# Kernel optimization log

Hardware: AMD Instinct MI355X
Metric: run time of the kernel (lower is better)

## Reference

```python
import jax, jax.numpy as jnp
import numpy as np

K = 1024
H = 16
HEAD = K // H

def setup_inputs() -> dict:
    key = jax.random.key(0)
    ks = jax.random.split(key, 6)
    b, t = 2, 2048
    x = jax.random.normal(ks[0], (b, t, K), dtype=jnp.float32)
    padding = jnp.ones((b, t), dtype=jnp.int32)
    s = 1.0 / np.sqrt(K)
    Wq = jax.random.normal(ks[1], (K, K), dtype=jnp.float32) * s
    Wk = jax.random.normal(ks[2], (K, K), dtype=jnp.float32) * s
    Wv = jax.random.normal(ks[3], (K, K), dtype=jnp.float32) * s
    Wo = jax.random.normal(ks[4], (K, K), dtype=jnp.float32) * s
    bo = jnp.zeros((K,), dtype=jnp.float32)
    return {"x": x, "padding": padding, "Wq": Wq, "Wk": Wk, "Wv": Wv, "Wo": Wo, "bo": bo}

def reference(x, padding, Wq, Wk, Wv, Wo, bo):
    b, t, k = x.shape
    h, d = H, HEAD
    # projections (nn.Linear: x @ W.T), then split heads -> [b,h,t,d]
    q = (x @ Wq.T).reshape(b, t, h, d).transpose(0, 2, 1, 3)
    kk = (x @ Wk.T).reshape(b, t, h, d).transpose(0, 2, 1, 3)
    v = (x @ Wv.T).reshape(b, t, h, d).transpose(0, 2, 1, 3)
    scores = jnp.einsum('bhqd,bhkd->bhqk', q, kk)
    # key-side padding mask: positions with padding==0 get -inf (before scaling,
    # same result since -inf/sqrt(d) == -inf)
    mask = (padding == 0)[:, None, None, :]  # [b,1,1,t]
    scores = jnp.where(mask, -jnp.inf, scores) / np.sqrt(d).astype(np.float32)
    weights = jax.nn.softmax(scores, axis=-1)
    out = jnp.einsum('bhqk,bhkd->bhqd', weights, v)
    out = out.transpose(0, 2, 1, 3).reshape(b, t, h * d)
    return out @ Wo.T + bo
```

## Files before the change

### kernel.cpp

```cpp
#include <hip/hip_runtime.h>
#include <cmath>
#include <stdint.h>

#define K_DIM 1024
#define NH    16
#define HD    64
#define T     2048
#define NTOK  4096
#define NBH   32

typedef __bf16 bf16x8 __attribute__((ext_vector_type(8)));
typedef float  f32x4  __attribute__((ext_vector_type(4)));

__device__ __forceinline__ unsigned short f2bf(float f) {
  union { float f; unsigned u; } v; v.f = f;
  unsigned u = v.u;
  return (unsigned short)((u + 0x7FFFu + ((u >> 16) & 1u)) >> 16);
}
__device__ __forceinline__ unsigned short f2bf_hu(float f) {
  union { float f; unsigned u; } v; v.f = f;
  return (unsigned short)((v.u + 0x8000u) >> 16);
}

__device__ __forceinline__ void gload16(const void* g, void* l) {
  __builtin_amdgcn_global_load_lds(
      (__attribute__((address_space(1))) void*)(g),
      (__attribute__((address_space(3))) void*)(l),
      16, 0, 0);
}

__global__ void convert_kernel(const float* __restrict__ x,
                               const float* __restrict__ Wq,
                               const float* __restrict__ Wk,
                               const float* __restrict__ Wv,
                               const float* __restrict__ Wo,
                               unsigned short* __restrict__ xb,
                               unsigned short* __restrict__ wqkv,
                               unsigned short* __restrict__ wob)
{
  const size_t NX = (size_t)NTOK * K_DIM;
  const size_t NW = (size_t)K_DIM * K_DIM;
  size_t i = ((size_t)blockIdx.x * blockDim.x + threadIdx.x) * 4;
  const float* src; unsigned short* dst; size_t off;
  float scale = 1.f;
  if (i < NX)             { src = x;  dst = xb;          off = i; }
  else if (i < NX + NW)   { src = Wq; dst = wqkv;        off = i - NX;
                            scale = 0.18033688011112042f; }
  else if (i < NX + 2*NW) { src = Wk; dst = wqkv + NW;   off = i - NX - NW; }
  else if (i < NX + 3*NW) { src = Wv; dst = wqkv + 2*NW; off = i - NX - 2*NW; }
  else                    { src = Wo; dst = wob;         off = i - NX - 3*NW; }
  float4 v = *(const float4*)(src + off);
  ushort4 o;
  o.x = f2bf(v.x * scale); o.y = f2bf(v.y * scale);
  o.z = f2bf(v.z * scale); o.w = f2bf(v.w * scale);
  *(ushort4*)(dst + off) = o;
}

template <int MODE, int TM, int TN>
__global__ __launch_bounds__(256, 2)
void gemm_bt(const unsigned short* __restrict__ A,
             const unsigned short* __restrict__ B,
             unsigned short* __restrict__ o_q,
             unsigned short* __restrict__ o_k,
             unsigned short* __restrict__ o_v,
             float* __restrict__ o_f,
             const float* __restrict__ bias)
{
  __shared__ unsigned short Asm[TM * 64];
  __shared__ unsigned short Bsm[TN * 64];
  const int tid  = threadIdx.x;
  const int wave = tid >> 6;
  const int lane = tid & 63;
  const int lq   = lane & 15;
  const int quad = lane >> 4;
  const int bm = blockIdx.x, bn = blockIdx.y;
  const int wm = (wave >> 1) * (TM / 2), wn = (wave & 1) * (TN / 2);
  const int MT = TM / 32, NT = TN / 32;

  f32x4 acc[MT][NT];
#pragma unroll
  for (int i = 0; i < MT; ++i)
#pragma unroll
    for (int j = 0; j < NT; ++j) acc[i][j] = (f32x4){0.f, 0.f, 0.f, 0.f};

  const char* Ab = (const char*)(A + (size_t)bm * TM * K_DIM);
  const char* Bb = (const char*)(B + (size_t)bn * TN * K_DIM);

  for (int k0 = 0; k0 < K_DIM; k0 += 64) {
#pragma unroll
    for (int i = 0; i < MT; ++i) {
      int off   = i * 4096 + wave * 1024 + lane * 16;
      int row   = off >> 7;
      int chunk = (off >> 4) & 7;
      int scol  = (chunk ^ (row & 7)) << 4;
      gload16(Ab + (size_t)row * (K_DIM * 2) + (size_t)k0 * 2 + scol,
              (char*)Asm + off - lane * 16);
    }
#pragma unroll
    for (int i = 0; i < NT; ++i) {
      int off   = i * 4096 + wave * 1024 + lane * 16;
      int row   = off >> 7;
      int chunk = (off >> 4) & 7;
      int scol  = (chunk ^ (row & 7)) << 4;
      gload16(Bb + (size_t)row * (K_DIM * 2) + (size_t)k0 * 2 + scol,
              (char*)Bsm + off - lane * 16);
    }
    __syncthreads();
#pragma unroll
    for (int kk = 0; kk < 64; kk += 32) {
      bf16x8 af[MT], bfr[NT];
#pragma unroll
      for (int mt = 0; mt < MT; ++mt) {
        int row = wm + mt * 16 + lq;
        int sw  = (quad + (kk >> 3)) ^ (row & 7);
        af[mt] = *(const bf16x8*)((const char*)Asm + row * 128 + (sw << 4));
      }
#pragma unroll
      for (int nt = 0; nt < NT; ++nt) {
        int row = wn + nt * 16 + lq;
        int sw  = (quad + (kk >> 3)) ^ (row & 7);
        bfr[nt] = *(const bf16x8*)((const char*)Bsm + row * 128 + (sw << 4));
      }
#pragma unroll
      for (int mt = 0; mt < MT; ++mt)
#pragma unroll
        for (int nt = 0; nt < NT; ++nt)
          acc[mt][nt] = __builtin_amdgcn_mfma_f32_16x16x32_bf16(af[mt], bfr[nt], acc[mt][nt], 0, 0, 0);
    }
    __syncthreads();
  }

#pragma unroll
  for (int mt = 0; mt < MT; ++mt) {
    int mbase = bm * TM + wm + mt * 16 + quad * 4;
#pragma unroll
    for (int nt = 0; nt < NT; ++nt) {
      int n = bn * TN + wn + nt * 16 + lq;
      if (MODE == 1) {
        int which = mbase >> 10, c = mbase & 1023;
        int h = c >> 6, d0 = c & 63;
        int b = n >> 11, t = n & 2047;
        if (which < 2) {
          ushort4 pk;
          pk.x = f2bf(acc[mt][nt][0]); pk.y = f2bf(acc[mt][nt][1]);
          pk.z = f2bf(acc[mt][nt][2]); pk.w = f2bf(acc[mt][nt][3]);
          unsigned short* dst = which ? o_k : o_q;
          *(ushort4*)&dst[((size_t)(b * NH + h) * T + t) * HD + d0] = pk;
        } else {
#pragma unroll
          for (int r = 0; r < 4; ++r)
            o_v[((size_t)(b * NH + h) * HD + d0 + r) * T + t] = f2bf(acc[mt][nt][r]);
        }
      } else {
        float4 bv = *(const float4*)&bias[mbase];
        float4 o;
        o.x = acc[mt][nt][0] + bv.x; o.y = acc[mt][nt][1] + bv.y;
        o.z = acc[mt][nt][2] + bv.z; o.w = acc[mt][nt][3] + bv.w;
        *(float4*)&o_f[(size_t)n * K_DIM + mbase] = o;
      }
    }
  }
}

__global__ __launch_bounds__(256, 2)
void attn_kernel(const unsigned short* __restrict__ Q,
                 const unsigned short* __restrict__ Kb,
                 const unsigned short* __restrict__ Vt,
                 const int* __restrict__ padding,
                 unsigned short* __restrict__ O)
{
  __shared__ unsigned short Ksm[128 * 64];
  __shared__ unsigned short Vsm[64 * 128];
  __shared__ unsigned short Plds[4][16 * 32 * 4];

  const int tid  = threadIdx.x;
  const int wave = tid >> 6;
  const int lane = tid & 63;
  const int lq   = lane & 15;
  const int quad = lane >> 4;
  const int bh = blockIdx.x;
  const int qt = blockIdx.y;
  const int b  = bh >> 4;
  const int h  = bh & 15;
  const int qbase = qt * 128 + wave * 32;

  bf16x8 qf[2][2];
#pragma unroll
  for (int nq = 0; nq < 2; ++nq)
#pragma unroll
    for (int kk = 0; kk < 2; ++kk)
      qf[nq][kk] = *(const bf16x8*)&Q[((size_t)bh * T + qbase + nq * 16 + lq) * HD + kk * 32 + quad * 8];

  f32x4 o_acc[4][2];
#pragma unroll
  for (int md = 0; md < 4; ++md)
#pragma unroll
    for (int nq = 0; nq < 2; ++nq) o_acc[md][nq] = (f32x4){0.f, 0.f, 0.f, 0.f};
  float l_part[2] = {0.f, 0.f};

  for (int kt = 0; kt < T / 128; ++kt) {
#pragma unroll
    for (int i = 0; i < 4; ++i) {
      int off = i * 4096 + wave * 1024 + lane * 16;
      {
        int row = off >> 7, chunk = (off >> 4) & 7;
        int scol = (chunk ^ (row & 7)) << 4;
        gload16((const char*)Kb + ((size_t)(bh * T + kt * 128 + row) * HD) * 2 + scol,
                (char*)Ksm + off - lane * 16);
      }
      {
        int row = off >> 8, chunk = (off >> 4) & 15;
        int scol = (chunk ^ (row & 15)) << 4;
        gload16((const char*)Vt + ((size_t)(bh * HD + row) * T + (size_t)kt * 128) * 2 + scol,
                (char*)Vsm + off - lane * 16);
      }
    }
    __syncthreads();

    f32x4 st[8][2];
#pragma unroll
    for (int nt = 0; nt < 8; ++nt)
#pragma unroll
      for (int nq = 0; nq < 2; ++nq) st[nt][nq] = (f32x4){0.f, 0.f, 0.f, 0.f};
#pragma unroll
    for (int kk = 0; kk < 2; ++kk) {
#pragma unroll
      for (int nt = 0; nt < 8; ++nt) {
        int row = nt * 16 + lq;
        int sw  = (quad + kk * 4) ^ (row & 7);
        bf16x8 kf = *(const bf16x8*)((const char*)Ksm + row * 128 + (sw << 4));
        st[nt][0] = __builtin_amdgcn_mfma_f32_16x16x32_bf16(kf, qf[0][kk], st[nt][0], 0, 0, 0);
        st[nt][1] = __builtin_amdgcn_mfma_f32_16x16x32_bf16(kf, qf[1][kk], st[nt][1], 0, 0, 0);
      }
    }

#pragma unroll
    for (int half = 0; half < 2; ++half) {
#pragma unroll
      for (int nt2 = 0; nt2 < 4; ++nt2) {
        int nt = half * 4 + nt2;
        int4 pd = *(const int4*)&padding[b * T + kt * 128 + nt * 16 + quad * 4];
#pragma unroll
        for (int nq = 0; nq < 2; ++nq) {
          float p0 = pd.x ? __builtin_amdgcn_exp2f(st[nt][nq][0]) : 0.f;
          float p1 = pd.y ? __builtin_amdgcn_exp2f(st[nt][nq][1]) : 0.f;
          float p2 = pd.z ? __builtin_amdgcn_exp2f(st[nt][nq][2]) : 0.f;
          float p3 = pd.w ? __builtin_amdgcn_exp2f(st[nt][nq][3]) : 0.f;
          l_part[nq] += (p0 + p1) + (p2 + p3);
          ushort4 pk;
          pk.x = f2bf_hu(p0); pk.y = f2bf_hu(p1); pk.z = f2bf_hu(p2); pk.w = f2bf_hu(p3);
          int row = nt2 * 4 + quad;
          int col = nq * 16 + lq;
          *(ushort4*)&Plds[wave][(row * 32 + col) * 4] = pk;
        }
      }
      asm volatile("s_waitcnt lgkmcnt(0)" ::: "memory");

#pragma unroll
      for (int kk2 = 0; kk2 < 2; ++kk2) {
        int kchunk = half * 2 + kk2;
        bf16x8 pf[2];
#pragma unroll
        for (int nq = 0; nq < 2; ++nq) {
          int row0 = kk2 * 8 + quad * 2;
          ushort4 lo = *(const ushort4*)&Plds[wave][((row0    ) * 32 + nq * 16 + lq) * 4];
          ushort4 hi = *(const ushort4*)&Plds[wave][((row0 + 1) * 32 + nq * 16 + lq) * 4];
          union { ushort4 u[2]; bf16x8 v; } cvt;
          cvt.u[0] = lo; cvt.u[1] = hi;
          pf[nq] = cvt.v;
        }
#pragma unroll
        for (int md = 0; md < 4; ++md) {
          int row = md * 16 + lq;
          int sw  = ((kchunk * 4 + quad) ^ (row & 15)) << 4;
          bf16x8 vf = *(const bf16x8*)((const char*)Vsm + row * 256 + sw);
          o_acc[md][0] = __builtin_amdgcn_mfma_f32_16x16x32_bf16(vf, pf[0], o_acc[md][0], 0, 0, 0);
          o_acc[md][1] = __builtin_amdgcn_mfma_f32_16x16x32_bf16(vf, pf[1], o_acc[md][1], 0, 0, 0);
        }
      }
      asm volatile("s_waitcnt lgkmcnt(0)" ::: "memory");
    }
    __syncthreads();
  }

  float inv[2];
#pragma unroll
  for (int nq = 0; nq < 2; ++nq) {
    float lsum = l_part[nq];
    lsum += __shfl_xor(lsum, 16);
    lsum += __shfl_xor(lsum, 32);
    inv[nq] = (lsum > 0.f) ? 1.f / lsum : 0.f;
  }
#pragma unroll
  for (int md = 0; md < 4; ++md) {
#pragma unroll
    for (int nq = 0; nq < 2; ++nq) {
      int t = qbase + nq * 16 + lq;
      int chan0 = h * HD + md * 16 + quad * 4;
      ushort4 pk;
      pk.x = f2bf(o_acc[md][nq][0] * inv[nq]);
      pk.y = f2bf(o_acc[md][nq][1] * inv[nq]);
      pk.z = f2bf(o_acc[md][nq][2] * inv[nq]);
      pk.w = f2bf(o_acc[md][nq][3] * inv[nq]);
      *(ushort4*)&O[((size_t)(b * T + t)) * K_DIM + chan0] = pk;
    }
  }
}

extern "C" void kernel_launch(void* const* d_in, const int* in_sizes, int n_in,
                              void* d_out, int out_size, void* d_ws, size_t ws_size,
                              hipStream_t stream)
{
  const float* x       = (const float*)d_in[0];
  const int*   padding = (const int*)d_in[1];
  const float* Wq      = (const float*)d_in[2];
  const float* Wk      = (const float*)d_in[3];
  const float* Wv      = (const float*)d_in[4];
  const float* Wo      = (const float*)d_in[5];
  const float* bo      = (const float*)d_in[6];
  float* out = (float*)d_out;

  char* ws = (char*)d_ws;
  unsigned short* xb   = (unsigned short*)(ws);
  unsigned short* wqkv = (unsigned short*)(ws + (8u  << 20));
  unsigned short* wob  = (unsigned short*)(ws + (14u << 20));
  unsigned short* qb   = (unsigned short*)(ws + (16u << 20));
  unsigned short* kb   = (unsigned short*)(ws + (24u << 20));
  unsigned short* vtb  = (unsigned short*)(ws + (32u << 20));
  unsigned short* ab   = (unsigned short*)(ws + (40u << 20));

  convert_kernel<<<8192, 256, 0, stream>>>(x, Wq, Wk, Wv, Wo, xb, wqkv, wob);

  gemm_bt<1, 128, 128><<<dim3(24, 32), 256, 0, stream>>>(wqkv, xb, qb, kb, vtb, nullptr, nullptr);

  attn_kernel<<<dim3(32, 16), 256, 0, stream>>>(qb, kb, vtb, padding, ab);

  gemm_bt<2, 64, 128><<<dim3(16, 32), 256, 0, stream>>>(wob, ab, nullptr, nullptr, nullptr, out, bo);
}
```

Baseline: 207.6 us.

## Use packed bf16 conversion, merge P staging, swap output GEMM operands, raise occupancy

Replaces the scalar float-to-bf16 rounding with the packed __float22bfloat162_rn intrinsic in the convert, projection, and attention epilogues. The attention kernel now computes the whole 128-key probability tile before one LDS wait and runs the PV MFMAs in a single pass, doubling the per-wave P buffer. The output projection swaps operands so tokens are the M dimension, with the grid changed to match and a strided scalar store epilogue. GEMM launch bounds go from 2 to 3 waves per SIMD, which may force register spilling or lower unroll quality.

```diff
diff --git a/kernel.cpp b/kernel.cpp
--- a/kernel.cpp
+++ b/kernel.cpp
@@ -1,4 +1,5 @@
 #include <hip/hip_runtime.h>
+#include <hip/hip_bf16.h>
 #include <cmath>
 #include <stdint.h>
 
@@ -17,9 +18,11 @@
   unsigned u = v.u;
   return (unsigned short)((u + 0x7FFFu + ((u >> 16) & 1u)) >> 16);
 }
-__device__ __forceinline__ unsigned short f2bf_hu(float f) {
-  union { float f; unsigned u; } v; v.f = f;
-  return (unsigned short)((v.u + 0x8000u) >> 16);
+__device__ __forceinline__ ushort4 pk4(float a, float b, float c, float d) {
+  union { __hip_bfloat162 h[2]; ushort4 u; } r;
+  r.h[0] = __float22bfloat162_rn(float2{a, b});
+  r.h[1] = __float22bfloat162_rn(float2{c, d});
+  return r.u;
 }
 
 __device__ __forceinline__ void gload16(const void* g, void* l) {
@@ -50,14 +53,11 @@
   else if (i < NX + 3*NW) { src = Wv; dst = wqkv + 2*NW; off = i - NX - 2*NW; }
   else                    { src = Wo; dst = wob;         off = i - NX - 3*NW; }
   float4 v = *(const float4*)(src + off);
-  ushort4 o;
-  o.x = f2bf(v.x * scale); o.y = f2bf(v.y * scale);
-  o.z = f2bf(v.z * scale); o.w = f2bf(v.w * scale);
-  *(ushort4*)(dst + off) = o;
+  *(ushort4*)(dst + off) = pk4(v.x * scale, v.y * scale, v.z * scale, v.w * scale);
 }
 
 template <int MODE, int TM, int TN>
-__global__ __launch_bounds__(256, 2)
+__global__ __launch_bounds__(256, 3)
 void gemm_bt(const unsigned short* __restrict__ A,
              const unsigned short* __restrict__ B,
              unsigned short* __restrict__ o_q,
@@ -141,9 +141,7 @@
         int h = c >> 6, d0 = c & 63;
         int b = n >> 11, t = n & 2047;
         if (which < 2) {
-          ushort4 pk;
-          pk.x = f2bf(acc[mt][nt][0]); pk.y = f2bf(acc[mt][nt][1]);
-          pk.z = f2bf(acc[mt][nt][2]); pk.w = f2bf(acc[mt][nt][3]);
+          ushort4 pk = pk4(acc[mt][nt][0], acc[mt][nt][1], acc[mt][nt][2], acc[mt][nt][3]);
           unsigned short* dst = which ? o_k : o_q;
           *(ushort4*)&dst[((size_t)(b * NH + h) * T + t) * HD + d0] = pk;
         } else {
@@ -152,11 +150,10 @@
             o_v[((size_t)(b * NH + h) * HD + d0 + r) * T + t] = f2bf(acc[mt][nt][r]);
         }
       } else {
-        float4 bv = *(const float4*)&bias[mbase];
-        float4 o;
-        o.x = acc[mt][nt][0] + bv.x; o.y = acc[mt][nt][1] + bv.y;
-        o.z = acc[mt][nt][2] + bv.z; o.w = acc[mt][nt][3] + bv.w;
-        *(float4*)&o_f[(size_t)n * K_DIM + mbase] = o;
+        float bv = bias[n];
+#pragma unroll
+        for (int r = 0; r < 4; ++r)
+          o_f[(size_t)(mbase + r) * K_DIM + n] = acc[mt][nt][r] + bv;
       }
     }
   }
@@ -171,7 +168,7 @@
 {
   __shared__ unsigned short Ksm[128 * 64];
   __shared__ unsigned short Vsm[64 * 128];
-  __shared__ unsigned short Plds[4][16 * 32 * 4];
+  __shared__ unsigned short Plds[4][32 * 32 * 4];
 
   const int tid  = threadIdx.x;
   const int wave = tid >> 6;
@@ -235,50 +232,42 @@
     }
 
 #pragma unroll
-    for (int half = 0; half < 2; ++half) {
-#pragma unroll
-      for (int nt2 = 0; nt2 < 4; ++nt2) {
-        int nt = half * 4 + nt2;
-        int4 pd = *(const int4*)&padding[b * T + kt * 128 + nt * 16 + quad * 4];
-#pragma unroll
-        for (int nq = 0; nq < 2; ++nq) {
-          float p0 = pd.x ? __builtin_amdgcn_exp2f(st[nt][nq][0]) : 0.f;
-          float p1 = pd.y ? __builtin_amdgcn_exp2f(st[nt][nq][1]) : 0.f;
-          float p2 = pd.z ? __builtin_amdgcn_exp2f(st[nt][nq][2]) : 0.f;
-          float p3 = pd.w ? __builtin_amdgcn_exp2f(st[nt][nq][3]) : 0.f;
-          l_part[nq] += (p0 + p1) + (p2 + p3);
-          ushort4 pk;
-          pk.x = f2bf_hu(p0); pk.y = f2bf_hu(p1); pk.z = f2bf_hu(p2); pk.w = f2bf_hu(p3);
-          int row = nt2 * 4 + quad;
-          int col = nq * 16 + lq;
-          *(ushort4*)&Plds[wave][(row * 32 + col) * 4] = pk;
-        }
-      }
-      asm volatile("s_waitcnt lgkmcnt(0)" ::: "memory");
-
-#pragma unroll
-      for (int kk2 = 0; kk2 < 2; ++kk2) {
-        int kchunk = half * 2 + kk2;
-        bf16x8 pf[2];
-#pragma unroll
-        for (int nq = 0; nq < 2; ++nq) {
-          int row0 = kk2 * 8 + quad * 2;
-          ushort4 lo = *(const ushort4*)&Plds[wave][((row0    ) * 32 + nq * 16 + lq) * 4];
-          ushort4 hi = *(const ushort4*)&Plds[wave][((row0 + 1) * 32 + nq * 16 + lq) * 4];
-          union { ushort4 u[2]; bf16x8 v; } cvt;
-          cvt.u[0] = lo; cvt.u[1] = hi;
-          pf[nq] = cvt.v;
-        }
-#pragma unroll
-        for (int md = 0; md < 4; ++md) {
-          int row = md * 16 + lq;
-          int sw  = ((kchunk * 4 + quad) ^ (row & 15)) << 4;
-          bf16x8 vf = *(const bf16x8*)((const char*)Vsm + row * 256 + sw);
-          o_acc[md][0] = __builtin_amdgcn_mfma_f32_16x16x32_bf16(vf, pf[0], o_acc[md][0], 0, 0, 0);
-          o_acc[md][1] = __builtin_amdgcn_mfma_f32_16x16x32_bf16(vf, pf[1], o_acc[md][1], 0, 0, 0);
-        }
-      }
-      asm volatile("s_waitcnt lgkmcnt(0)" ::: "memory");
+    for (int nt = 0; nt < 8; ++nt) {
+      int4 pd = *(const int4*)&padding[b * T + kt * 128 + nt * 16 + quad * 4];
+#pragma unroll
+      for (int nq = 0; nq < 2; ++nq) {
+        float p0 = pd.x ? __builtin_amdgcn_exp2f(st[nt][nq][0]) : 0.f;
+        float p1 = pd.y ? __builtin_amdgcn_exp2f(st[nt][nq][1]) : 0.f;
+        float p2 = pd.z ? __builtin_amdgcn_exp2f(st[nt][nq][2]) : 0.f;
+        float p3 = pd.w ? __builtin_amdgcn_exp2f(st[nt][nq][3]) : 0.f;
+        l_part[nq] += (p0 + p1) + (p2 + p3);
+        int row = nt * 4 + quad;
+        int col = nq * 16 + lq;
+        *(ushort4*)&Plds[wave][(row * 32 + col) * 4] = pk4(p0, p1, p2, p3);
+      }
+    }
+    asm volatile("s_waitcnt lgkmcnt(0)" ::: "memory");
+
+#pragma unroll
+    for (int kk = 0; kk < 4; ++kk) {
+      bf16x8 pf[2];
+#pragma unroll
+      for (int nq = 0; nq < 2; ++nq) {
+        int row0 = kk * 8 + quad * 2;
+        ushort4 lo = *(const ushort4*)&Plds[wave][((row0    ) * 32 + nq * 16 + lq) * 4];
+        ushort4 hi = *(const ushort4*)&Plds[wave][((row0 + 1) * 32 + nq * 16 + lq) * 4];
+        union { ushort4 u[2]; bf16x8 v; } cvt;
+        cvt.u[0] = lo; cvt.u[1] = hi;
+        pf[nq] = cvt.v;
+      }
+#pragma unroll
+      for (int md = 0; md < 4; ++md) {
+        int row = md * 16 + lq;
+        int sw  = ((kk * 4 + quad) ^ (row & 15)) << 4;
+        bf16x8 vf = *(const bf16x8*)((const char*)Vsm + row * 256 + sw);
+        o_acc[md][0] = __builtin_amdgcn_mfma_f32_16x16x32_bf16(vf, pf[0], o_acc[md][0], 0, 0, 0);
+        o_acc[md][1] = __builtin_amdgcn_mfma_f32_16x16x32_bf16(vf, pf[1], o_acc[md][1], 0, 0, 0);
+      }
     }
     __syncthreads();
   }
@@ -297,12 +286,9 @@
     for (int nq = 0; nq < 2; ++nq) {
       int t = qbase + nq * 16 + lq;
       int chan0 = h * HD + md * 16 + quad * 4;
-      ushort4 pk;
-      pk.x = f2bf(o_acc[md][nq][0] * inv[nq]);
-      pk.y = f2bf(o_acc[md][nq][1] * inv[nq]);
-      pk.z = f2bf(o_acc[md][nq][2] * inv[nq]);
-      pk.w = f2bf(o_acc[md][nq][3] * inv[nq]);
-      *(ushort4*)&O[((size_t)(b * T + t)) * K_DIM + chan0] = pk;
+      *(ushort4*)&O[((size_t)(b * T + t)) * K_DIM + chan0] =
+          pk4(o_acc[md][nq][0] * inv[nq], o_acc[md][nq][1] * inv[nq],
+              o_acc[md][nq][2] * inv[nq], o_acc[md][nq][3] * inv[nq]);
     }
   }
 }
@@ -335,5 +321,5 @@
 
   attn_kernel<<<dim3(32, 16), 256, 0, stream>>>(qb, kb, vtb, padding, ab);
 
-  gemm_bt<2, 64, 128><<<dim3(16, 32), 256, 0, stream>>>(wob, ab, nullptr, nullptr, nullptr, out, bo);
-}
+  gemm_bt<2, 64, 128><<<dim3(64, 8), 256, 0, stream>>>(ab, wob, nullptr, nullptr, nullptr, out, bo);
+}
```

Measured after the change: 194.8 us. 1.07x faster.
